# Performance work log

Hardware: AMD Instinct MI355X
Metric: run time of the kernel (lower is better)

The kernel has to match this reference:

```python
import jax, jax.numpy as jnp
import numpy as np

GAMMA = 1.0
EPS = 1e-8


def setup_inputs() -> dict:
    key = jax.random.key(0)
    k1, k2 = jax.random.split(key)
    inputs = jax.random.normal(k1, (16, 2048, 1024), dtype=jnp.float32)
    codebook = jax.random.normal(k2, (2048, 1024), dtype=jnp.float32)  # normal(1.0) init
    return {"inputs": inputs, "codebook": codebook}


def reference(inputs, codebook):
    # inputs: [B, T, D]; codebook: [K, D]
    features = jax.lax.stop_gradient(inputs)
    # similarity = sum over D of features[..., None, :] * codebook -> [B, T, K]
    similarity = jnp.einsum('btd,kd->btk', features, codebook)
    scores = jax.nn.softmax(similarity, axis=-1)  # [B, T, K]
    nn_idx = jnp.argmax(scores, axis=-1)  # [B, T]
    # one_hot(nn_idx) @ codebook == direct gather
    quantized = codebook[nn_idx]  # [B, T, D]
    quantized = quantized - jnp.mean(quantized, axis=-1, keepdims=True)
    quantized = quantized / jnp.linalg.norm(quantized, axis=-1, keepdims=True)
    # entropy loss
    flat = scores.reshape(-1, scores.shape[-1])  # [B*T, K]
    h_clust = -jnp.mean(jnp.sum(flat * jnp.log2(flat + EPS), axis=-1))
    diversity = jnp.mean(flat, axis=0)  # [K]
    h_diversity = -jnp.sum(diversity * jnp.log2(diversity + EPS))
    loss = h_clust - GAMMA * h_diversity
    quantization_loss = jnp.full(scores.shape, loss)  # [B, T, K], scalar broadcast
    # straight-through estimator
    quantized = inputs + jax.lax.stop_gradient(quantized - inputs)
    return (quantized, quantization_loss, nn_idx, codebook)
```

## Files before the change

### kernel.cpp

```cpp
#include <hip/hip_runtime.h>
#include <math.h>

#define M_TOTAL 32768
#define D_DIM   1024
#define K_DIM   2048

#define OUT0_OFF 0ULL
#define OUT1_OFF 33554432ULL
#define OUT2_OFF 100663296ULL
#define OUT3_OFF 100696064ULL

typedef _Float16 f16x4 __attribute__((ext_vector_type(4)));
typedef _Float16 f16x8 __attribute__((ext_vector_type(8)));
typedef float    f32x4 __attribute__((ext_vector_type(4)));

#define STR_(x) #x
#define STR(x) STR_(x)
#define WAITVM(N) asm volatile("s_waitcnt vmcnt(" STR(N) ")" ::: "memory")

__device__ __forceinline__ void async_copy16(void* lds, const void* g) {
    __builtin_amdgcn_global_load_lds(
        (const __attribute__((address_space(1))) unsigned int*)g,
        (__attribute__((address_space(3))) unsigned int*)lds, 16, 0, 0);
}

__global__ __launch_bounds__(256) void convcb_kernel(const float* __restrict__ C,
                                                     _Float16* __restrict__ ch,
                                                     _Float16* __restrict__ cl) {
    const int i = blockIdx.x * 256 + threadIdx.x;
    const float4 c = ((const float4*)C)[i];
    f16x4 h, l;
    h.x = (_Float16)c.x; l.x = (_Float16)(c.x - (float)h.x);
    h.y = (_Float16)c.y; l.y = (_Float16)(c.y - (float)h.y);
    h.z = (_Float16)c.z; l.z = (_Float16)(c.z - (float)h.z);
    h.w = (_Float16)c.w; l.w = (_Float16)(c.w - (float)h.w);
    ((f16x4*)ch)[i] = h;
    ((f16x4*)cl)[i] = l;
}

__global__ __launch_bounds__(256) void convx_kernel(const float* __restrict__ X,
                                                    _Float16* __restrict__ xh) {
    const size_t i = (size_t)blockIdx.x * 256 + threadIdx.x;
    const float4 a = ((const float4*)X)[i];
    f16x4 h;
    h.x = (_Float16)a.x; h.y = (_Float16)a.y;
    h.z = (_Float16)a.z; h.w = (_Float16)a.w;
    ((f16x4*)xh)[i] = h;
}

__device__ __forceinline__ void loadA8(f16x8* a, const _Float16* Ab, int wm, int fr, int fq) {
#pragma unroll
    for (int kh = 0; kh < 2; kh++)
#pragma unroll
        for (int mi = 0; mi < 4; mi++) {
            const int row = wm + mi * 16 + fr;
            a[kh * 4 + mi] = *(const f16x8*)(Ab + kh * 8192 + row * 32 + (fq ^ ((row >> 1) & 3)) * 8);
        }
}
__device__ __forceinline__ void loadB8(f16x8* b, const _Float16* Bb, int wn, int fr, int fq) {
#pragma unroll
    for (int kh = 0; kh < 2; kh++)
#pragma unroll
        for (int ni = 0; ni < 4; ni++) {
            const int row = wn + ni * 16 + fr;
            b[kh * 4 + ni] = *(const f16x8*)(Bb + kh * 4096 + row * 32 + (fq ^ ((row >> 1) & 3)) * 8);
        }
}

__global__ __launch_bounds__(512, 2) void gemm_kernel(const _Float16* __restrict__ XH,
                                                      const _Float16* __restrict__ CH,
                                                      const _Float16* __restrict__ CL,
                                                      float* __restrict__ S) {
    __shared__ _Float16 lds[65536];
    _Float16* const A0  = lds;
    _Float16* const Bh0 = lds + 16384;
    _Float16* const Bl0 = lds + 24576;
    _Float16* const A1  = lds + 32768;
    _Float16* const Bh1 = lds + 49152;
    _Float16* const Bl1 = lds + 57344;

    const int tid  = threadIdx.x;
    const int lane = tid & 63;
    const int wave = tid >> 6;

    const int bq  = blockIdx.x;
    const int xcd = bq & 7;
    const int idx = bq >> 3;
    const int m0 = (xcd * 16 + (idx >> 4)) * 256;
    const int n0 = (idx & 15) * 128;

    const int wm = (wave & 3) * 64;
    const int wn = (wave >> 2) * 64;
    const int fr = lane & 15;
    const int fq = lane >> 4;

    size_t aoff[2][2]; int alds[2][2];
#pragma unroll
    for (int e = 0; e < 2; e++) {
        const int U = (wave * 2 + e) * 64 + lane;
        const int row = U >> 2;
#pragma unroll
        for (int kh = 0; kh < 2; kh++) {
            aoff[e][kh] = (size_t)(m0 + row) * D_DIM + (size_t)(kh * 4 + ((U & 3) ^ ((row >> 1) & 3))) * 8;
            alds[e][kh] = kh * 8192 + (wave * 2 + e) * 512;
        }
    }
    size_t boff[2]; int blds[2];
    {
        const int U = wave * 64 + lane;
        const int row = U >> 2;
#pragma unroll
        for (int kh = 0; kh < 2; kh++) {
            boff[kh] = (size_t)(n0 + row) * D_DIM + (size_t)(kh * 4 + ((U & 3) ^ ((row >> 1) & 3))) * 8;
            blds[kh] = kh * 4096 + wave * 512;
        }
    }

#define STAGE_C0(Abuf, Bbuf, kb) do {                                                       \
    async_copy16((void*)((Abuf) + alds[0][0]), (const void*)(XH + aoff[0][0] + (kb)));      \
    async_copy16((void*)((Abuf) + alds[1][0]), (const void*)(XH + aoff[1][0] + (kb)));      \
    async_copy16((void*)((Abuf) + alds[0][1]), (const void*)(XH + aoff[0][1] + (kb)));      \
    async_copy16((void*)((Abuf) + alds[1][1]), (const void*)(XH + aoff[1][1] + (kb)));      \
    async_copy16((void*)((Bbuf) + blds[0]),    (const void*)(CH + boff[0] + (kb)));         \
    async_copy16((void*)((Bbuf) + blds[1]),    (const void*)(CH + boff[1] + (kb)));         \
} while (0)
#define STAGE_C1(Bbuf, kb) do {                                                             \
    async_copy16((void*)((Bbuf) + blds[0]),    (const void*)(CL + boff[0] + (kb)));         \
    async_copy16((void*)((Bbuf) + blds[1]),    (const void*)(CL + boff[1] + (kb)));         \
} while (0)

#define PH32() do {                                                                         \
    __builtin_amdgcn_s_barrier();                                                           \
    asm volatile("s_waitcnt lgkmcnt(0)" ::: "memory");                                      \
    __builtin_amdgcn_sched_barrier(0);                                                      \
    __builtin_amdgcn_s_setprio(1);                                                          \
    _Pragma("unroll")                                                                       \
    for (int kh = 0; kh < 2; kh++) {                                                        \
        _Pragma("unroll")                                                                   \
        for (int mi = 0; mi < 4; mi++) {                                                    \
            _Pragma("unroll")                                                               \
            for (int ni = 0; ni < 4; ni++)                                                  \
                acc[mi][ni] = __builtin_amdgcn_mfma_f32_16x16x32_f16(a[kh * 4 + mi], b[kh * 4 + ni], acc[mi][ni], 0, 0, 0); \
        }                                                                                   \
    }                                                                                       \
    __builtin_amdgcn_s_setprio(0);                                                          \
    __builtin_amdgcn_s_barrier();                                                           \
} while (0)

    f32x4 acc[4][4];
#pragma unroll
    for (int mi = 0; mi < 4; mi++)
#pragma unroll
        for (int ni = 0; ni < 4; ni++) {
            acc[mi][ni].x = 0.f; acc[mi][ni].y = 0.f;
            acc[mi][ni].z = 0.f; acc[mi][ni].w = 0.f;
        }

    f16x8 a[8], b[8];

    STAGE_C0(A0, Bh0, 0);
    STAGE_C1(Bl0, 0);
    WAITVM(2);
    __builtin_amdgcn_s_barrier();

    for (int t = 0; t < 15; t++) {
        _Float16* const Ac  = (t & 1) ? A1 : A0;
        _Float16* const Bhc = (t & 1) ? Bh1 : Bh0;
        _Float16* const Blc = (t & 1) ? Bl1 : Bl0;
        _Float16* const An  = (t & 1) ? A0 : A1;
        _Float16* const Bhn = (t & 1) ? Bh0 : Bh1;
        _Float16* const Bln = (t & 1) ? Bl0 : Bl1;
        const size_t kb = (size_t)(t + 1) * 64;

        loadA8(a, Ac, wm, fr, fq);
        loadB8(b, Bhc, wn, fr, fq);
        STAGE_C0(An, Bhn, kb);
        WAITVM(6);
        PH32();
        loadB8(b, Blc, wn, fr, fq);
        STAGE_C1(Bln, kb);
        WAITVM(2);
        PH32();
    }

    loadA8(a, A1, wm, fr, fq);
    loadB8(b, Bh1, wn, fr, fq);
    WAITVM(0);
    PH32();
    loadB8(b, Bl1, wn, fr, fq);
    asm volatile("s_waitcnt lgkmcnt(0)" ::: "memory");
    __builtin_amdgcn_sched_barrier(0);
#pragma unroll
    for (int kh = 0; kh < 2; kh++)
#pragma unroll
        for (int mi = 0; mi < 4; mi++)
#pragma unroll
            for (int ni = 0; ni < 4; ni++)
                acc[mi][ni] = __builtin_amdgcn_mfma_f32_16x16x32_f16(a[kh * 4 + mi], b[kh * 4 + ni], acc[mi][ni], 0, 0, 0);

#pragma unroll
    for (int mi = 0; mi < 4; mi++)
#pragma unroll
        for (int r = 0; r < 4; r++) {
            float* dst = S + (size_t)(m0 + wm + mi * 16 + fq * 4 + r) * K_DIM + n0 + wn;
#pragma unroll
            for (int ni = 0; ni < 4; ni++) dst[ni * 16 + fr] = acc[mi][ni][r];
        }
#undef STAGE_C0
#undef STAGE_C1
#undef PH32
}

#define MARGIN 0.125f
__global__ __launch_bounds__(256) void statsref_kernel(const float* __restrict__ S,
                                                       const float* __restrict__ X,
                                                       const float* __restrict__ C,
                                                       float* __restrict__ div_acc,
                                                       float* __restrict__ hclust_acc,
                                                       float* __restrict__ nn_out,
                                                       float* __restrict__ out0) {
    __shared__ float sdiv[K_DIM];
    __shared__ int scnt[32];
    __shared__ int scand[32][8];
    const int tid = threadIdx.x;
    for (int k = tid; k < K_DIM; k += 256) sdiv[k] = 0.0f;
    if (tid < 32) scnt[tid] = 0;
    __syncthreads();

    const int lane = tid & 63;
    const int wave = tid >> 6;

    float dreg[32];
#pragma unroll
    for (int j = 0; j < 32; j++) dreg[j] = 0.0f;
    float ent_acc = 0.0f;

    for (int r8 = 0; r8 < 8; r8++) {
        const int lr = wave * 8 + r8;
        const int row = blockIdx.x * 32 + lr;
        const float* srow = S + (size_t)row * K_DIM;

        float v[32];
#pragma unroll
        for (int j = 0; j < 32; j++) v[j] = srow[lane + 64 * j];

        float m = v[0];
#pragma unroll
        for (int j = 1; j < 32; j++) m = fmaxf(m, v[j]);
        for (int off = 32; off > 0; off >>= 1) m = fmaxf(m, __shfl_xor(m, off, 64));

        const float thresh = m - MARGIN;
#pragma unroll
        for (int j = 0; j < 32; j++) {
            if (v[j] > thresh) {
                const int slot = atomicAdd(&scnt[lr], 1);
                if (slot < 8) scand[lr][slot] = lane + 64 * j;
            }
        }

        float Z = 0.0f;
#pragma unroll
        for (int j = 0; j < 32; j++) {
            v[j] = __expf(v[j] - m);
            Z += v[j];
        }
        for (int off = 32; off > 0; off >>= 1) Z += __shfl_xor(Z, off, 64);
        const float invZ = 1.0f / Z;

#pragma unroll
        for (int j = 0; j < 32; j++) {
            const float p = v[j] * invZ;
            dreg[j] += p;
            ent_acc += p * __log2f(p + 1e-8f);
        }
    }

#pragma unroll
    for (int j = 0; j < 32; j++) atomicAdd(&sdiv[lane + 64 * j], dreg[j]);
    for (int off = 32; off > 0; off >>= 1) ent_acc += __shfl_xor(ent_acc, off, 64);
    if (lane == 0) atomicAdd(hclust_acc, ent_acc);
    __syncthreads();

    for (int k = tid; k < K_DIM; k += 256) atomicAdd(&div_acc[k], sdiv[k]);

    for (int r8 = 0; r8 < 8; r8++) {
        const int lr = wave * 8 + r8;
        const int row = blockIdx.x * 32 + lr;
        const int n = min(scnt[lr], 8);
        const float* x = X + (size_t)row * D_DIM;

        float4 xv[4];
#pragma unroll
        for (int q = 0; q < 4; q++) xv[q] = *(const float4*)(x + lane * 4 + 256 * q);

        double bestv = -1.0e300;
        int besti = 0x7fffffff;
        for (int c = 0; c < n; c++) {
            const int cidx = scand[lr][c];
            const float* cb = C + (size_t)cidx * D_DIM;
            double s = 0.0;
#pragma unroll
            for (int q = 0; q < 4; q++) {
                const float4 cv = *(const float4*)(cb + lane * 4 + 256 * q);
                s += (double)xv[q].x * cv.x + (double)xv[q].y * cv.y +
                     (double)xv[q].z * cv.z + (double)xv[q].w * cv.w;
            }
            for (int off = 32; off > 0; off >>= 1) s += __shfl_xor(s, off, 64);
            if (s > bestv || (s == bestv && cidx < besti)) { bestv = s; besti = cidx; }
        }
        if (lane == 0) nn_out[row] = (float)besti;

        const float* c = C + (size_t)besti * D_DIM;
        float4 v[4];
        float sum = 0.0f;
#pragma unroll
        for (int q = 0; q < 4; q++) {
            v[q] = *(const float4*)(c + lane * 4 + 256 * q);
            sum += v[q].x + v[q].y + v[q].z + v[q].w;
        }
        for (int off = 32; off > 0; off >>= 1) sum += __shfl_xor(sum, off, 64);
        const float mean = sum * (1.0f / 1024.0f);

        float ss = 0.0f;
#pragma unroll
        for (int q = 0; q < 4; q++) {
            v[q].x -= mean; v[q].y -= mean; v[q].z -= mean; v[q].w -= mean;
            ss += v[q].x * v[q].x + v[q].y * v[q].y + v[q].z * v[q].z + v[q].w * v[q].w;
        }
        for (int off = 32; off > 0; off >>= 1) ss += __shfl_xor(ss, off, 64);
        const float inv = 1.0f / sqrtf(ss);

        float* o = out0 + (size_t)row * D_DIM;
#pragma unroll
        for (int q = 0; q < 4; q++) {
            float4 w = v[q];
            w.x *= inv; w.y *= inv; w.z *= inv; w.w *= inv;
            *(float4*)(o + lane * 4 + 256 * q) = w;
        }
    }
}

__global__ __launch_bounds__(256) void finalize_kernel(const float* __restrict__ div_acc,
                                                       const float* __restrict__ hclust_acc,
                                                       float* __restrict__ loss_out) {
    __shared__ float red[256];
    const int tid = threadIdx.x;
    float sum = 0.0f;
    for (int k = tid; k < K_DIM; k += 256) {
        const float d = div_acc[k] * (1.0f / 32768.0f);
        sum += d * __log2f(d + 1e-8f);
    }
    red[tid] = sum;
    __syncthreads();
    for (int s = 128; s > 0; s >>= 1) {
        if (tid < s) red[tid] += red[tid + s];
        __syncthreads();
    }
    if (tid == 0) {
        const float h_clust = -hclust_acc[0] * (1.0f / 32768.0f);
        const float h_div = -red[0];
        loss_out[0] = h_clust - 1.0f * h_div;
    }
}

__global__ __launch_bounds__(256) void fill_kernel(float* __restrict__ out1,
                                                   const float* __restrict__ loss_ptr) {
    const float v = loss_ptr[0];
    const float4 f = make_float4(v, v, v, v);
    float4* o = (float4*)out1;
    const size_t stride = (size_t)gridDim.x * blockDim.x;
    for (size_t i = (size_t)blockIdx.x * blockDim.x + threadIdx.x; i < 16777216ULL; i += stride)
        o[i] = f;
}

__global__ __launch_bounds__(256) void copycb_kernel(const float* __restrict__ C,
                                                     float* __restrict__ out3) {
    const size_t i = (size_t)blockIdx.x * 256 + threadIdx.x;
    if (i < 524288ULL) ((float4*)out3)[i] = ((const float4*)C)[i];
}

extern "C" void kernel_launch(void* const* d_in, const int* in_sizes, int n_in,
                              void* d_out, int out_size, void* d_ws, size_t ws_size,
                              hipStream_t stream) {
    const float* X = (const float*)d_in[0];
    const float* C = (const float*)d_in[1];
    float* out = (float*)d_out;

    char* scratch = (char*)d_out;
    _Float16* CH  = (_Float16*)(scratch);
    _Float16* CL  = (_Float16*)(scratch + (4 << 20));
    _Float16* XH  = (_Float16*)(scratch + (16 << 20));

    char* s3 = (char*)(out + OUT3_OFF);
    float* div_acc = (float*)s3;
    float* hclust  = div_acc + 2048;
    float* loss    = div_acc + 2049;

    float* S = out + OUT1_OFF;

    hipMemsetAsync(s3, 0, 8192 + 16, stream);

    convcb_kernel<<<2048, 256, 0, stream>>>(C, CH, CL);

    convx_kernel<<<32768, 256, 0, stream>>>(X, XH);

    gemm_kernel<<<2048, 512, 0, stream>>>(XH, CH, CL, S);

    statsref_kernel<<<M_TOTAL / 32, 256, 0, stream>>>(S, X, C, div_acc, hclust,
                                                      out + OUT2_OFF, out + OUT0_OFF);

    finalize_kernel<<<1, 256, 0, stream>>>(div_acc, hclust, loss);

    fill_kernel<<<8192, 256, 0, stream>>>(out + OUT1_OFF, loss);

    copycb_kernel<<<2048, 256, 0, stream>>>(C, out + OUT3_OFF);
}
```

Before: 913.3 us.

## Halve GEMM K-step for higher occupancy, fuse conversions, closed-form entropy

The GEMM now stages 32-wide K slices instead of 64, which halves LDS use and the A/B register fragments and raises the launch bound to 4 blocks per CU. In exchange it runs twice as many barrier-separated phases. The codebook and input fp16 conversion kernels are merged into one launch. The per-row entropy is computed in closed form as sum(e*d)/Z - log2 Z, which drops the per-element log2. That closed form omits the epsilon term inside the log.

```diff
diff --git a/kernel.cpp b/kernel.cpp
--- a/kernel.cpp
+++ b/kernel.cpp
@@ -24,60 +24,57 @@
         (__attribute__((address_space(3))) unsigned int*)lds, 16, 0, 0);
 }
 
-__global__ __launch_bounds__(256) void convcb_kernel(const float* __restrict__ C,
-                                                     _Float16* __restrict__ ch,
-                                                     _Float16* __restrict__ cl) {
-    const int i = blockIdx.x * 256 + threadIdx.x;
-    const float4 c = ((const float4*)C)[i];
-    f16x4 h, l;
-    h.x = (_Float16)c.x; l.x = (_Float16)(c.x - (float)h.x);
-    h.y = (_Float16)c.y; l.y = (_Float16)(c.y - (float)h.y);
-    h.z = (_Float16)c.z; l.z = (_Float16)(c.z - (float)h.z);
-    h.w = (_Float16)c.w; l.w = (_Float16)(c.w - (float)h.w);
-    ((f16x4*)ch)[i] = h;
-    ((f16x4*)cl)[i] = l;
-}
-
-__global__ __launch_bounds__(256) void convx_kernel(const float* __restrict__ X,
-                                                    _Float16* __restrict__ xh) {
-    const size_t i = (size_t)blockIdx.x * 256 + threadIdx.x;
-    const float4 a = ((const float4*)X)[i];
-    f16x4 h;
-    h.x = (_Float16)a.x; h.y = (_Float16)a.y;
-    h.z = (_Float16)a.z; h.w = (_Float16)a.w;
-    ((f16x4*)xh)[i] = h;
-}
-
-__device__ __forceinline__ void loadA8(f16x8* a, const _Float16* Ab, int wm, int fr, int fq) {
-#pragma unroll
-    for (int kh = 0; kh < 2; kh++)
-#pragma unroll
-        for (int mi = 0; mi < 4; mi++) {
-            const int row = wm + mi * 16 + fr;
-            a[kh * 4 + mi] = *(const f16x8*)(Ab + kh * 8192 + row * 32 + (fq ^ ((row >> 1) & 3)) * 8);
-        }
-}
-__device__ __forceinline__ void loadB8(f16x8* b, const _Float16* Bb, int wn, int fr, int fq) {
-#pragma unroll
-    for (int kh = 0; kh < 2; kh++)
-#pragma unroll
-        for (int ni = 0; ni < 4; ni++) {
-            const int row = wn + ni * 16 + fr;
-            b[kh * 4 + ni] = *(const f16x8*)(Bb + kh * 4096 + row * 32 + (fq ^ ((row >> 1) & 3)) * 8);
-        }
-}
-
-__global__ __launch_bounds__(512, 2) void gemm_kernel(const _Float16* __restrict__ XH,
+__global__ __launch_bounds__(256) void conv_kernel(const float* __restrict__ C,
+                                                   _Float16* __restrict__ ch,
+                                                   _Float16* __restrict__ cl,
+                                                   const float* __restrict__ X,
+                                                   _Float16* __restrict__ xh) {
+    if (blockIdx.x < 2048) {
+        const int i = blockIdx.x * 256 + threadIdx.x;
+        const float4 c = ((const float4*)C)[i];
+        f16x4 h, l;
+        h.x = (_Float16)c.x; l.x = (_Float16)(c.x - (float)h.x);
+        h.y = (_Float16)c.y; l.y = (_Float16)(c.y - (float)h.y);
+        h.z = (_Float16)c.z; l.z = (_Float16)(c.z - (float)h.z);
+        h.w = (_Float16)c.w; l.w = (_Float16)(c.w - (float)h.w);
+        ((f16x4*)ch)[i] = h;
+        ((f16x4*)cl)[i] = l;
+    } else {
+        const size_t i = (size_t)(blockIdx.x - 2048) * 256 + threadIdx.x;
+        const float4 a = ((const float4*)X)[i];
+        f16x4 h;
+        h.x = (_Float16)a.x; h.y = (_Float16)a.y;
+        h.z = (_Float16)a.z; h.w = (_Float16)a.w;
+        ((f16x4*)xh)[i] = h;
+    }
+}
+
+__device__ __forceinline__ void loadA4(f16x8* a, const _Float16* Ab, int wm, int fr, int fq) {
+#pragma unroll
+    for (int mi = 0; mi < 4; mi++) {
+        const int row = wm + mi * 16 + fr;
+        a[mi] = *(const f16x8*)(Ab + row * 32 + (fq ^ ((row >> 1) & 3)) * 8);
+    }
+}
+__device__ __forceinline__ void loadB4(f16x8* b, const _Float16* Bb, int wn, int fr, int fq) {
+#pragma unroll
+    for (int ni = 0; ni < 4; ni++) {
+        const int row = wn + ni * 16 + fr;
+        b[ni] = *(const f16x8*)(Bb + row * 32 + (fq ^ ((row >> 1) & 3)) * 8);
+    }
+}
+
+__global__ __launch_bounds__(512, 4) void gemm_kernel(const _Float16* __restrict__ XH,
                                                       const _Float16* __restrict__ CH,
                                                       const _Float16* __restrict__ CL,
                                                       float* __restrict__ S) {
-    __shared__ _Float16 lds[65536];
+    __shared__ _Float16 lds[32768];
     _Float16* const A0  = lds;
-    _Float16* const Bh0 = lds + 16384;
-    _Float16* const Bl0 = lds + 24576;
-    _Float16* const A1  = lds + 32768;
-    _Float16* const Bh1 = lds + 49152;
-    _Float16* const Bl1 = lds + 57344;
+    _Float16* const Bh0 = lds + 8192;
+    _Float16* const Bl0 = lds + 12288;
+    _Float16* const A1  = lds + 16384;
+    _Float16* const Bh1 = lds + 24576;
+    _Float16* const Bl1 = lds + 28672;
 
     const int tid  = threadIdx.x;
     const int lane = tid & 63;
@@ -94,57 +91,43 @@
     const int fr = lane & 15;
     const int fq = lane >> 4;
 
-    size_t aoff[2][2]; int alds[2][2];
+    size_t aoff[2]; int alds[2];
 #pragma unroll
     for (int e = 0; e < 2; e++) {
         const int U = (wave * 2 + e) * 64 + lane;
         const int row = U >> 2;
-#pragma unroll
-        for (int kh = 0; kh < 2; kh++) {
-            aoff[e][kh] = (size_t)(m0 + row) * D_DIM + (size_t)(kh * 4 + ((U & 3) ^ ((row >> 1) & 3))) * 8;
-            alds[e][kh] = kh * 8192 + (wave * 2 + e) * 512;
-        }
-    }
-    size_t boff[2]; int blds[2];
+        aoff[e] = (size_t)(m0 + row) * D_DIM + (size_t)((U & 3) ^ ((row >> 1) & 3)) * 8;
+        alds[e] = (wave * 2 + e) * 512;
+    }
+    size_t boff; int blds;
     {
         const int U = wave * 64 + lane;
         const int row = U >> 2;
-#pragma unroll
-        for (int kh = 0; kh < 2; kh++) {
-            boff[kh] = (size_t)(n0 + row) * D_DIM + (size_t)(kh * 4 + ((U & 3) ^ ((row >> 1) & 3))) * 8;
-            blds[kh] = kh * 4096 + wave * 512;
-        }
-    }
-
-#define STAGE_C0(Abuf, Bbuf, kb) do {                                                       \
-    async_copy16((void*)((Abuf) + alds[0][0]), (const void*)(XH + aoff[0][0] + (kb)));      \
-    async_copy16((void*)((Abuf) + alds[1][0]), (const void*)(XH + aoff[1][0] + (kb)));      \
-    async_copy16((void*)((Abuf) + alds[0][1]), (const void*)(XH + aoff[0][1] + (kb)));      \
-    async_copy16((void*)((Abuf) + alds[1][1]), (const void*)(XH + aoff[1][1] + (kb)));      \
-    async_copy16((void*)((Bbuf) + blds[0]),    (const void*)(CH + boff[0] + (kb)));         \
-    async_copy16((void*)((Bbuf) + blds[1]),    (const void*)(CH + boff[1] + (kb)));         \
+        boff = (size_t)(n0 + row) * D_DIM + (size_t)((U & 3) ^ ((row >> 1) & 3)) * 8;
+        blds = wave * 512;
+    }
+
+#define STAGE_C0(Abuf, Bbuf, kb) do {                                                   \
+    async_copy16((void*)((Abuf) + alds[0]), (const void*)(XH + aoff[0] + (kb)));        \
+    async_copy16((void*)((Abuf) + alds[1]), (const void*)(XH + aoff[1] + (kb)));        \
+    async_copy16((void*)((Bbuf) + blds),    (const void*)(CH + boff + (kb)));           \
 } while (0)
-#define STAGE_C1(Bbuf, kb) do {                                                             \
-    async_copy16((void*)((Bbuf) + blds[0]),    (const void*)(CL + boff[0] + (kb)));         \
-    async_copy16((void*)((Bbuf) + blds[1]),    (const void*)(CL + boff[1] + (kb)));         \
-} while (0)
-
-#define PH32() do {                                                                         \
-    __builtin_amdgcn_s_barrier();                                                           \
-    asm volatile("s_waitcnt lgkmcnt(0)" ::: "memory");                                      \
-    __builtin_amdgcn_sched_barrier(0);                                                      \
-    __builtin_amdgcn_s_setprio(1);                                                          \
-    _Pragma("unroll")                                                                       \
-    for (int kh = 0; kh < 2; kh++) {                                                        \
-        _Pragma("unroll")                                                                   \
-        for (int mi = 0; mi < 4; mi++) {                                                    \
-            _Pragma("unroll")                                                               \
-            for (int ni = 0; ni < 4; ni++)                                                  \
-                acc[mi][ni] = __builtin_amdgcn_mfma_f32_16x16x32_f16(a[kh * 4 + mi], b[kh * 4 + ni], acc[mi][ni], 0, 0, 0); \
-        }                                                                                   \
-    }                                                                                       \
-    __builtin_amdgcn_s_setprio(0);                                                          \
-    __builtin_amdgcn_s_barrier();                                                           \
+#define STAGE_C1(Bbuf, kb) \
+    async_copy16((void*)((Bbuf) + blds),    (const void*)(CL + boff + (kb)))
+
+#define PH16() do {                                                                     \
+    __builtin_amdgcn_s_barrier();                                                       \
+    asm volatile("s_waitcnt lgkmcnt(0)" ::: "memory");                                  \
+    __builtin_amdgcn_sched_barrier(0);                                                  \
+    __builtin_amdgcn_s_setprio(1);                                                      \
+    _Pragma("unroll")                                                                   \
+    for (int mi = 0; mi < 4; mi++) {                                                    \
+        _Pragma("unroll")                                                               \
+        for (int ni = 0; ni < 4; ni++)                                                  \
+            acc[mi][ni] = __builtin_amdgcn_mfma_f32_16x16x32_f16(a[mi], b[ni], acc[mi][ni], 0, 0, 0); \
+    }                                                                                   \
+    __builtin_amdgcn_s_setprio(0);                                                      \
+    __builtin_amdgcn_s_barrier();                                                       \
 } while (0)
 
     f32x4 acc[4][4];
@@ -156,47 +139,45 @@
             acc[mi][ni].z = 0.f; acc[mi][ni].w = 0.f;
         }
 
-    f16x8 a[8], b[8];
+    f16x8 a[4], b[4];
 
     STAGE_C0(A0, Bh0, 0);
     STAGE_C1(Bl0, 0);
-    WAITVM(2);
+    WAITVM(1);
     __builtin_amdgcn_s_barrier();
 
-    for (int t = 0; t < 15; t++) {
+    for (int t = 0; t < 31; t++) {
         _Float16* const Ac  = (t & 1) ? A1 : A0;
         _Float16* const Bhc = (t & 1) ? Bh1 : Bh0;
         _Float16* const Blc = (t & 1) ? Bl1 : Bl0;
         _Float16* const An  = (t & 1) ? A0 : A1;
         _Float16* const Bhn = (t & 1) ? Bh0 : Bh1;
         _Float16* const Bln = (t & 1) ? Bl0 : Bl1;
-        const size_t kb = (size_t)(t + 1) * 64;
-
-        loadA8(a, Ac, wm, fr, fq);
-        loadB8(b, Bhc, wn, fr, fq);
+        const size_t kb = (size_t)(t + 1) * 32;
+
+        loadA4(a, Ac, wm, fr, fq);
+        loadB4(b, Bhc, wn, fr, fq);
         STAGE_C0(An, Bhn, kb);
-        WAITVM(6);
-        PH32();
-        loadB8(b, Blc, wn, fr, fq);
+        WAITVM(3);
+        PH16();
+        loadB4(b, Blc, wn, fr, fq);
         STAGE_C1(Bln, kb);
-        WAITVM(2);
-        PH32();
-    }
-
-    loadA8(a, A1, wm, fr, fq);
-    loadB8(b, Bh1, wn, fr, fq);
+        WAITVM(1);
+        PH16();
+    }
+
+    loadA4(a, A1, wm, fr, fq);
+    loadB4(b, Bh1, wn, fr, fq);
     WAITVM(0);
-    PH32();
-    loadB8(b, Bl1, wn, fr, fq);
+    PH16();
+    loadB4(b, Bl1, wn, fr, fq);
     asm volatile("s_waitcnt lgkmcnt(0)" ::: "memory");
     __builtin_amdgcn_sched_barrier(0);
 #pragma unroll
-    for (int kh = 0; kh < 2; kh++)
-#pragma unroll
-        for (int mi = 0; mi < 4; mi++)
-#pragma unroll
-            for (int ni = 0; ni < 4; ni++)
-                acc[mi][ni] = __builtin_amdgcn_mfma_f32_16x16x32_f16(a[kh * 4 + mi], b[kh * 4 + ni], acc[mi][ni], 0, 0, 0);
+    for (int mi = 0; mi < 4; mi++)
+#pragma unroll
+        for (int ni = 0; ni < 4; ni++)
+            acc[mi][ni] = __builtin_amdgcn_mfma_f32_16x16x32_f16(a[mi], b[ni], acc[mi][ni], 0, 0, 0);
 
 #pragma unroll
     for (int mi = 0; mi < 4; mi++)
@@ -208,7 +189,7 @@
         }
 #undef STAGE_C0
 #undef STAGE_C1
-#undef PH32
+#undef PH16
 }
 
 #define MARGIN 0.125f
@@ -258,26 +239,28 @@
             }
         }
 
-        float Z = 0.0f;
+        float Z = 0.0f, E2 = 0.0f;
 #pragma unroll
         for (int j = 0; j < 32; j++) {
-            v[j] = __expf(v[j] - m);
-            Z += v[j];
-        }
-        for (int off = 32; off > 0; off >>= 1) Z += __shfl_xor(Z, off, 64);
+            const float d = v[j] - m;
+            const float e = __expf(d);
+            v[j] = e;
+            Z += e;
+            E2 += e * d;
+        }
+        for (int off = 32; off > 0; off >>= 1) {
+            Z  += __shfl_xor(Z, off, 64);
+            E2 += __shfl_xor(E2, off, 64);
+        }
         const float invZ = 1.0f / Z;
 
 #pragma unroll
-        for (int j = 0; j < 32; j++) {
-            const float p = v[j] * invZ;
-            dreg[j] += p;
-            ent_acc += p * __log2f(p + 1e-8f);
-        }
+        for (int j = 0; j < 32; j++) dreg[j] += v[j] * invZ;
+        ent_acc += 1.4426950408889634f * E2 * invZ - __log2f(Z);
     }
 
 #pragma unroll
     for (int j = 0; j < 32; j++) atomicAdd(&sdiv[lane + 64 * j], dreg[j]);
-    for (int off = 32; off > 0; off >>= 1) ent_acc += __shfl_xor(ent_acc, off, 64);
     if (lane == 0) atomicAdd(hclust_acc, ent_acc);
     __syncthreads();
 
@@ -400,9 +383,7 @@
 
     hipMemsetAsync(s3, 0, 8192 + 16, stream);
 
-    convcb_kernel<<<2048, 256, 0, stream>>>(C, CH, CL);
-
-    convx_kernel<<<32768, 256, 0, stream>>>(X, XH);
+    conv_kernel<<<34816, 256, 0, stream>>>(C, CH, CL, X, XH);
 
     gemm_kernel<<<2048, 512, 0, stream>>>(XH, CH, CL, S);
 
```

Measured after the change: 867.4 us. 5.0% less time.
